# Optimization experiments

Measured on AMD Instinct MI355X. Metric: run time of the kernel, lower is better.

The kernel has to match this reference:

```python
import jax, jax.numpy as jnp
import numpy as np

B, S, D, H = 2, 4096, 256, 4
DH = D // H  # head dim = 64


def setup_inputs() -> dict:
    key = jax.random.key(0)
    ks = jax.random.split(key, 7)
    scale = 1.0 / np.sqrt(D)
    return {
        "x": jax.random.normal(ks[0], (B, S, D), dtype=jnp.float32),
        "Wq": jax.random.normal(ks[1], (D, D), dtype=jnp.float32) * scale,
        "bq": jax.random.normal(ks[2], (D,), dtype=jnp.float32) * scale,
        "Wk": jax.random.normal(ks[3], (D, D), dtype=jnp.float32) * scale,
        "bk": jax.random.normal(ks[4], (D,), dtype=jnp.float32) * scale,
        "Wv": jax.random.normal(ks[5], (D, D), dtype=jnp.float32) * scale,
        "bv": jax.random.normal(ks[6], (D,), dtype=jnp.float32) * scale,
    }


def reference(x, Wq, bq, Wk, bk, Wv, bv):
    b, s, d = x.shape
    # torch Linear: y = x @ W.T + b ; W stored as [out, in]
    q = (jnp.einsum('bsd,ed->bse', x, Wq) + bq).reshape(b, s, H, DH)
    k = (jnp.einsum('bsd,ed->bse', x, Wk) + bk).reshape(b, s, H, DH)
    v = (jnp.einsum('bsd,ed->bse', x, Wv) + bv).reshape(b, s, H, DH)
    # scores: [b, s(query), t(key), h]
    scores = jnp.einsum('bshd,bthd->bsth', q, k) / jnp.sqrt(jnp.float32(DH))
    # softmax over key axis t (dim=-2 in torch layout bsth)
    weights = jax.nn.softmax(scores, axis=2)
    out = jnp.einsum('bsth,bthd->bshd', weights, v)
    return out.reshape(b, s, d)
```

## Files before the change

kernel.cpp:

```cpp
#include <hip/hip_runtime.h>

#define S_LEN 4096
#define D_MODEL 256
#define NH 4
#define DH 64
#define CSC 0.18033688011112042f

typedef __attribute__((ext_vector_type(8))) short bf16x8;
typedef __attribute__((ext_vector_type(8))) unsigned short u16x8;
typedef __attribute__((ext_vector_type(4))) float f32x4;
typedef __attribute__((ext_vector_type(16))) float f32x16;
typedef __attribute__((ext_vector_type(2))) unsigned int u32x2;
typedef __attribute__((ext_vector_type(4))) unsigned int u32x4;

#define MFMA16(a, b, c) __builtin_amdgcn_mfma_f32_16x16x32_bf16((a), (b), (c), 0, 0, 0)
#define MFMA32(a, b, c) __builtin_amdgcn_mfma_f32_32x32x16_bf16((a), (b), (c), 0, 0, 0)
#define SWZ(r, c) ((c) ^ (((r) & 7) << 3))

static __device__ __forceinline__ unsigned short f2bf(float f) {
  unsigned int u = __float_as_uint(f);
  u += 0x7fffu + ((u >> 16) & 1u);
  return (unsigned short)(u >> 16);
}

static __device__ __forceinline__ unsigned int pack2(float lo, float hi) {
  return ((unsigned int)f2bf(hi) << 16) | (unsigned int)f2bf(lo);
}

static __device__ __forceinline__ unsigned int cvtpk(float lo, float hi) {
  unsigned int r;
  asm("v_cvt_pk_bf16_f32 %0, %1, %2" : "=v"(r) : "v"(lo), "v"(hi));
  return r;
}

static __device__ __forceinline__ u16x8 cvt8(float4 a, float4 b) {
  u16x8 v;
  v[0] = f2bf(a.x); v[1] = f2bf(a.y); v[2] = f2bf(a.z); v[3] = f2bf(a.w);
  v[4] = f2bf(b.x); v[5] = f2bf(b.y); v[6] = f2bf(b.z); v[7] = f2bf(b.w);
  return v;
}

__global__ __launch_bounds__(256) void prep(
    const float* __restrict__ Wq, const float* __restrict__ Wk,
    const float* __restrict__ Wv, unsigned short* __restrict__ Wb)
{
  const int gid = blockIdx.x * 256 + threadIdx.x;
  const int l   = gid & 63;
  const int f   = gid >> 6;
  const int kk  = f & 7;
  const int ctn = f >> 3;
  const int ct  = ctn & 3, nt = ctn >> 2;
  const int pj  = nt >> 2, h = nt & 3;
  const float* Wsel = (pj == 0) ? Wq : (pj == 1) ? Wk : Wv;
  const float* src =
      Wsel + (size_t)(h * 64 + ct * 16 + (l & 15)) * D_MODEL + kk * 32 + (l >> 4) * 8;
  float4 a = *(const float4*)src;
  float4 b = *(const float4*)(src + 4);
  *(u16x8*)(Wb + (size_t)gid * 8) = cvt8(a, b);
}

__global__ __launch_bounds__(256) void qkv_proj(
    const float* __restrict__ x, const unsigned short* __restrict__ Wb,
    const float* __restrict__ bq, const float* __restrict__ bk,
    const float* __restrict__ bv,
    unsigned short* __restrict__ Qh, unsigned short* __restrict__ Kh,
    unsigned short* __restrict__ Vt)
{
  __shared__ unsigned short xs[32][264];

  const int tid  = threadIdx.x;
  const int lane = tid & 63;
  const int w    = tid >> 6;
  const int r16  = lane & 15;
  const int hi   = lane >> 4;
  const int m0   = (blockIdx.x >> 1) * 32;
  const int ntB  = (blockIdx.x & 1) * 6;

  {
    const int r  = tid >> 3;
    const int c0 = (tid & 7) * 32;
    const float* xp = x + (size_t)(m0 + r) * D_MODEL + c0;
#pragma unroll
    for (int i = 0; i < 32; i += 8) {
      float4 a = *(const float4*)(xp + i);
      float4 b = *(const float4*)(xp + i + 4);
      *(u16x8*)&xs[r][c0 + i] = cvt8(a, b);
    }
  }
  __syncthreads();

  const int bb = m0 >> 12;
  const int s_base = m0 & 4095;

#pragma unroll
  for (int t = 0; t < 6; ++t) {
    const int nt = ntB + t, pj = nt >> 2, h = nt & 3;
    f32x4 acc[2] = {};
    const size_t fb = (size_t)(nt * 4 + w) * 8;
#pragma unroll
    for (int kk = 0; kk < 8; ++kk) {
      bf16x8 bw = *(const bf16x8*)(Wb + (fb + kk) * 512 + lane * 8);
#pragma unroll
      for (int rt = 0; rt < 2; ++rt) {
        bf16x8 af = *(const bf16x8*)&xs[rt * 16 + r16][kk * 32 + hi * 8];
        acc[rt] = MFMA16(af, bw, acc[rt]);
      }
    }
    const float* bsel = (pj == 0) ? bq : (pj == 1) ? bk : bv;
    const float bias = bsel[h * 64 + w * 16 + r16];

    if (pj < 2) {
      unsigned short* dst = (pj == 0) ? Qh : Kh;
      const float sc = (pj == 0) ? CSC : 1.0f;
#pragma unroll
      for (int rt = 0; rt < 2; ++rt)
#pragma unroll
        for (int j = 0; j < 4; ++j) {
          int s = s_base + rt * 16 + hi * 4 + j;
          dst[((size_t)(bb * NH + h) * S_LEN + s) * DH + w * 16 + r16] =
              f2bf((acc[rt][j] + bias) * sc);
        }
    } else {
      unsigned short* dst = Vt + ((size_t)(bb * NH + h) * DH + w * 16 + r16) * S_LEN;
#pragma unroll
      for (int rt = 0; rt < 2; ++rt) {
        int s0 = s_base + rt * 16 + hi * 4;
        uint2 uu;
        uu.x = pack2(acc[rt][0] + bias, acc[rt][1] + bias);
        uu.y = pack2(acc[rt][2] + bias, acc[rt][3] + bias);
        *(uint2*)(dst + s0) = uu;
      }
    }
  }
}

__global__ __launch_bounds__(512) void attn(
    const unsigned short* __restrict__ Qh,
    const unsigned short* __restrict__ Kh,
    const unsigned short* __restrict__ Vt,
    float* __restrict__ out)
{
  __shared__ unsigned short Ks[2][2][64][64];
  __shared__ unsigned short Vs[2][2][64][64];

  const int tid = threadIdx.x;
  const int ln  = tid & 63;
  const int wv  = tid >> 6;
  const int g   = wv >> 2;
  const int wq  = wv & 3;
  const int r32 = ln & 31;
  const int h   = ln >> 5;

  const int bid = blockIdx.x;
  const int bh  = bid & 7;
  const int q0  = (bid >> 3) * 128;

  const unsigned short* Qb = Qh + (size_t)bh * S_LEN * DH;
  const unsigned short* Kb = Kh + (size_t)bh * S_LEN * DH;
  const unsigned short* Vb = Vt + (size_t)bh * DH * S_LEN;

  const int q = q0 + wq * 32 + r32;
  bf16x8 qf[4];
#pragma unroll
  for (int s = 0; s < 4; ++s)
    qf[s] = *(const bf16x8*)(Qb + (size_t)q * DH + s * 16 + h * 8);

  f32x16 o0 = {}, o1 = {};
  float l_run = 0.f;

  const int p  = tid >> 8;
  const int u  = tid & 255;
  const int sr = u >> 2;
  const int sc = (u & 3) * 16;

  uint4 kA, kB, vA, vB;
  {
    const unsigned short* kp = Kb + ((size_t)(p * 64 + sr)) * DH + sc;
    kA = *(const uint4*)kp;  kB = *(const uint4*)(kp + 8);
    const unsigned short* vp = Vb + (size_t)sr * S_LEN + p * 64 + sc;
    vA = *(const uint4*)vp;  vB = *(const uint4*)(vp + 8);
  }
  *(uint4*)&Ks[0][p][sr][SWZ(sr, sc)]     = kA;
  *(uint4*)&Ks[0][p][sr][SWZ(sr, sc + 8)] = kB;
  *(uint4*)&Vs[0][p][sr][SWZ(sr, sc)]     = vA;
  *(uint4*)&Vs[0][p][sr][SWZ(sr, sc + 8)] = vB;
  {
    const int c = 2 + p;
    const unsigned short* kp = Kb + ((size_t)(c * 64 + sr)) * DH + sc;
    kA = *(const uint4*)kp;  kB = *(const uint4*)(kp + 8);
    const unsigned short* vp = Vb + (size_t)sr * S_LEN + c * 64 + sc;
    vA = *(const uint4*)vp;  vB = *(const uint4*)(vp + 8);
  }

  for (int it = 0; it < 32; ++it) {
    __syncthreads();
    if (it < 31) {
      const int nb = (it + 1) & 1;
      *(uint4*)&Ks[nb][p][sr][SWZ(sr, sc)]     = kA;
      *(uint4*)&Ks[nb][p][sr][SWZ(sr, sc + 8)] = kB;
      *(uint4*)&Vs[nb][p][sr][SWZ(sr, sc)]     = vA;
      *(uint4*)&Vs[nb][p][sr][SWZ(sr, sc + 8)] = vB;
      int c = 2 * (it + 2) + p;  if (c > 63) c = 63;
      const unsigned short* kp = Kb + ((size_t)(c * 64 + sr)) * DH + sc;
      kA = *(const uint4*)kp;  kB = *(const uint4*)(kp + 8);
      const unsigned short* vp = Vb + (size_t)sr * S_LEN + c * 64 + sc;
      vA = *(const uint4*)vp;  vB = *(const uint4*)(vp + 8);
    }
    const int tb = it & 1;

    f32x16 s0 = {}, s1 = {};
    __builtin_amdgcn_s_setprio(1);
#pragma unroll
    for (int s = 0; s < 4; ++s) {
      bf16x8 a0 = *(const bf16x8*)&Ks[tb][g][r32][SWZ(r32, s * 16 + h * 8)];
      bf16x8 a1 = *(const bf16x8*)&Ks[tb][g][32 + r32][SWZ(r32, s * 16 + h * 8)];
      s0 = MFMA32(a0, qf[s], s0);
      s1 = MFMA32(a1, qf[s], s1);
    }
    __builtin_amdgcn_s_setprio(0);

    float ps = 0.f;
#pragma unroll
    for (int i = 0; i < 16; ++i) {
      s0[i] = __builtin_amdgcn_exp2f(s0[i]);  ps += s0[i];
      s1[i] = __builtin_amdgcn_exp2f(s1[i]);  ps += s1[i];
    }
    l_run += ps;

    unsigned int u0[8], u1[8];
#pragma unroll
    for (int gg = 0; gg < 4; ++gg) {
      u0[gg * 2 + 0] = cvtpk(s0[4 * gg + 0], s0[4 * gg + 1]);
      u0[gg * 2 + 1] = cvtpk(s0[4 * gg + 2], s0[4 * gg + 3]);
      u1[gg * 2 + 0] = cvtpk(s1[4 * gg + 0], s1[4 * gg + 1]);
      u1[gg * 2 + 1] = cvtpk(s1[4 * gg + 2], s1[4 * gg + 3]);
    }
    bf16x8 pb[4];
#pragma unroll
    for (int S = 0; S < 2; ++S) {
      u32x2 w0 = __builtin_amdgcn_permlane32_swap(u0[4 * S + 0], u0[4 * S + 2], false, false);
      u32x2 w1 = __builtin_amdgcn_permlane32_swap(u0[4 * S + 1], u0[4 * S + 3], false, false);
      u32x4 t0; t0[0] = w0[0]; t0[1] = w1[0]; t0[2] = w0[1]; t0[3] = w1[1];
      pb[S] = __builtin_bit_cast(bf16x8, t0);
      u32x2 w2 = __builtin_amdgcn_permlane32_swap(u1[4 * S + 0], u1[4 * S + 2], false, false);
      u32x2 w3 = __builtin_amdgcn_permlane32_swap(u1[4 * S + 1], u1[4 * S + 3], false, false);
      u32x4 t1; t1[0] = w2[0]; t1[1] = w3[0]; t1[2] = w2[1]; t1[3] = w3[1];
      pb[2 + S] = __builtin_bit_cast(bf16x8, t1);
    }

    __builtin_amdgcn_s_setprio(1);
#pragma unroll
    for (int s = 0; s < 4; ++s) {
      bf16x8 a0 = *(const bf16x8*)&Vs[tb][g][r32][SWZ(r32, s * 16 + h * 8)];
      bf16x8 a1 = *(const bf16x8*)&Vs[tb][g][32 + r32][SWZ(r32, s * 16 + h * 8)];
      o0 = MFMA32(a0, pb[s], o0);
      o1 = MFMA32(a1, pb[s], o1);
    }
    __builtin_amdgcn_s_setprio(0);
  }

  __syncthreads();
  float* cb = (float*)&Ks[0][0][0][0];
  const int cbase = wq * 64 + ln;
  if (g == 1) {
#pragma unroll
    for (int i = 0; i < 16; ++i) cb[i * 256 + cbase] = o0[i];
    cb[16 * 256 + cbase] = l_run;
  }
  __syncthreads();
  if (g == 0) {
#pragma unroll
    for (int i = 0; i < 16; ++i) o0[i] += cb[i * 256 + cbase];
    l_run += cb[16 * 256 + cbase];
  }
  __syncthreads();
  if (g == 1) {
#pragma unroll
    for (int i = 0; i < 16; ++i) cb[i * 256 + cbase] = o1[i];
  }
  __syncthreads();
  if (g == 0) {
#pragma unroll
    for (int i = 0; i < 16; ++i) o1[i] += cb[i * 256 + cbase];

    const float lt  = l_run + __shfl_xor(l_run, 32);
    const float inv = 1.f / lt;
    const int bb = bh >> 2, hd = bh & 3;
    float* op = out + ((size_t)(bb * S_LEN + q)) * D_MODEL + hd * DH;
#pragma unroll
    for (int gg = 0; gg < 4; ++gg) {
      float4 v0, v1;
      v0.x = o0[4 * gg + 0] * inv;  v0.y = o0[4 * gg + 1] * inv;
      v0.z = o0[4 * gg + 2] * inv;  v0.w = o0[4 * gg + 3] * inv;
      *(float4*)(op + 8 * gg + 4 * h) = v0;
      v1.x = o1[4 * gg + 0] * inv;  v1.y = o1[4 * gg + 1] * inv;
      v1.z = o1[4 * gg + 2] * inv;  v1.w = o1[4 * gg + 3] * inv;
      *(float4*)(op + 32 + 8 * gg + 4 * h) = v1;
    }
  }
}

extern "C" void kernel_launch(void* const* d_in, const int* in_sizes, int n_in,
                              void* d_out, int out_size, void* d_ws, size_t ws_size,
                              hipStream_t stream) {
  const float* x  = (const float*)d_in[0];
  const float* Wq = (const float*)d_in[1];
  const float* bq = (const float*)d_in[2];
  const float* Wk = (const float*)d_in[3];
  const float* bk = (const float*)d_in[4];
  const float* Wv = (const float*)d_in[5];
  const float* bv = (const float*)d_in[6];
  float* out = (float*)d_out;

  const size_t per = (size_t)2 * NH * S_LEN * DH;
  if (ws_size < 3 * per * sizeof(unsigned short)) return;
  unsigned short* Qh = (unsigned short*)d_ws;
  unsigned short* Kh = Qh + per;
  unsigned short* Vt = Kh + per;
  unsigned short* Wb = (unsigned short*)d_out;

  prep<<<96, 256, 0, stream>>>(Wq, Wk, Wv, Wb);
  qkv_proj<<<512, 256, 0, stream>>>(x, Wb, bq, bk, bv, Qh, Kh, Vt);
  attn<<<256, 512, 0, stream>>>(Qh, Kh, Vt, out);
}
```

Before: 66.98 us.

## Split attention KV loop across four wave groups with 1024-thread blocks

Doubles the attention block to 1024 threads so four wave groups each process a quarter of the key/value tiles, halving the per-group loop trip count. K/V staging moves into one combined shared buffer, and each thread now loads a single tile per stage. The final cross-group reduction becomes a two-level tree through shared memory with a padded stride of 33 floats to avoid bank conflicts. This adds waves to hide latency, at the cost of more register pressure under the 1024-thread launch bound and a longer reduction at the end.

```diff
diff --git a/kernel.cpp b/kernel.cpp
--- a/kernel.cpp
+++ b/kernel.cpp
@@ -134,14 +134,13 @@
   }
 }
 
-__global__ __launch_bounds__(512) void attn(
+__global__ __launch_bounds__(1024) void attn(
     const unsigned short* __restrict__ Qh,
     const unsigned short* __restrict__ Kh,
     const unsigned short* __restrict__ Vt,
     float* __restrict__ out)
 {
-  __shared__ unsigned short Ks[2][2][64][64];
-  __shared__ unsigned short Vs[2][2][64][64];
+  __shared__ unsigned short KVs[2][2][4][64][64];
 
   const int tid = threadIdx.x;
   const int ln  = tid & 63;
@@ -168,39 +167,38 @@
   f32x16 o0 = {}, o1 = {};
   float l_run = 0.f;
 
-  const int p  = tid >> 8;
   const int u  = tid & 255;
   const int sr = u >> 2;
   const int sc = (u & 3) * 16;
 
   uint4 kA, kB, vA, vB;
   {
-    const unsigned short* kp = Kb + ((size_t)(p * 64 + sr)) * DH + sc;
+    const unsigned short* kp = Kb + ((size_t)(g * 64 + sr)) * DH + sc;
     kA = *(const uint4*)kp;  kB = *(const uint4*)(kp + 8);
-    const unsigned short* vp = Vb + (size_t)sr * S_LEN + p * 64 + sc;
+    const unsigned short* vp = Vb + (size_t)sr * S_LEN + g * 64 + sc;
     vA = *(const uint4*)vp;  vB = *(const uint4*)(vp + 8);
   }
-  *(uint4*)&Ks[0][p][sr][SWZ(sr, sc)]     = kA;
-  *(uint4*)&Ks[0][p][sr][SWZ(sr, sc + 8)] = kB;
-  *(uint4*)&Vs[0][p][sr][SWZ(sr, sc)]     = vA;
-  *(uint4*)&Vs[0][p][sr][SWZ(sr, sc + 8)] = vB;
+  *(uint4*)&KVs[0][0][g][sr][SWZ(sr, sc)]     = kA;
+  *(uint4*)&KVs[0][0][g][sr][SWZ(sr, sc + 8)] = kB;
+  *(uint4*)&KVs[1][0][g][sr][SWZ(sr, sc)]     = vA;
+  *(uint4*)&KVs[1][0][g][sr][SWZ(sr, sc + 8)] = vB;
   {
-    const int c = 2 + p;
+    const int c = 4 + g;
     const unsigned short* kp = Kb + ((size_t)(c * 64 + sr)) * DH + sc;
     kA = *(const uint4*)kp;  kB = *(const uint4*)(kp + 8);
     const unsigned short* vp = Vb + (size_t)sr * S_LEN + c * 64 + sc;
     vA = *(const uint4*)vp;  vB = *(const uint4*)(vp + 8);
   }
 
-  for (int it = 0; it < 32; ++it) {
+  for (int it = 0; it < 16; ++it) {
     __syncthreads();
-    if (it < 31) {
+    if (it < 15) {
       const int nb = (it + 1) & 1;
-      *(uint4*)&Ks[nb][p][sr][SWZ(sr, sc)]     = kA;
-      *(uint4*)&Ks[nb][p][sr][SWZ(sr, sc + 8)] = kB;
-      *(uint4*)&Vs[nb][p][sr][SWZ(sr, sc)]     = vA;
-      *(uint4*)&Vs[nb][p][sr][SWZ(sr, sc + 8)] = vB;
-      int c = 2 * (it + 2) + p;  if (c > 63) c = 63;
+      *(uint4*)&KVs[0][nb][g][sr][SWZ(sr, sc)]     = kA;
+      *(uint4*)&KVs[0][nb][g][sr][SWZ(sr, sc + 8)] = kB;
+      *(uint4*)&KVs[1][nb][g][sr][SWZ(sr, sc)]     = vA;
+      *(uint4*)&KVs[1][nb][g][sr][SWZ(sr, sc + 8)] = vB;
+      int c = 4 * (it + 2) + g;  if (c > 63) c = 63;
       const unsigned short* kp = Kb + ((size_t)(c * 64 + sr)) * DH + sc;
       kA = *(const uint4*)kp;  kB = *(const uint4*)(kp + 8);
       const unsigned short* vp = Vb + (size_t)sr * S_LEN + c * 64 + sc;
@@ -212,8 +210,8 @@
     __builtin_amdgcn_s_setprio(1);
 #pragma unroll
     for (int s = 0; s < 4; ++s) {
-      bf16x8 a0 = *(const bf16x8*)&Ks[tb][g][r32][SWZ(r32, s * 16 + h * 8)];
-      bf16x8 a1 = *(const bf16x8*)&Ks[tb][g][32 + r32][SWZ(r32, s * 16 + h * 8)];
+      bf16x8 a0 = *(const bf16x8*)&KVs[0][tb][g][r32][SWZ(r32, s * 16 + h * 8)];
+      bf16x8 a1 = *(const bf16x8*)&KVs[0][tb][g][32 + r32][SWZ(r32, s * 16 + h * 8)];
       s0 = MFMA32(a0, qf[s], s0);
       s1 = MFMA32(a1, qf[s], s1);
     }
@@ -251,8 +249,8 @@
     __builtin_amdgcn_s_setprio(1);
 #pragma unroll
     for (int s = 0; s < 4; ++s) {
-      bf16x8 a0 = *(const bf16x8*)&Vs[tb][g][r32][SWZ(r32, s * 16 + h * 8)];
-      bf16x8 a1 = *(const bf16x8*)&Vs[tb][g][32 + r32][SWZ(r32, s * 16 + h * 8)];
+      bf16x8 a0 = *(const bf16x8*)&KVs[1][tb][g][r32][SWZ(r32, s * 16 + h * 8)];
+      bf16x8 a1 = *(const bf16x8*)&KVs[1][tb][g][32 + r32][SWZ(r32, s * 16 + h * 8)];
       o0 = MFMA32(a0, pb[s], o0);
       o1 = MFMA32(a1, pb[s], o1);
     }
@@ -260,28 +258,35 @@
   }
 
   __syncthreads();
-  float* cb = (float*)&Ks[0][0][0][0];
+  float* cb = (float*)&KVs[0][0][0][0][0];
   const int cbase = wq * 64 + ln;
+
+  if (g >= 2) {
+    const int base = ((g - 2) * 256 + cbase) * 33;
+#pragma unroll
+    for (int i = 0; i < 16; ++i) { cb[base + i] = o0[i]; cb[base + 16 + i] = o1[i]; }
+    cb[base + 32] = l_run;
+  }
+  __syncthreads();
+  if (g < 2) {
+    const int base = (g * 256 + cbase) * 33;
+#pragma unroll
+    for (int i = 0; i < 16; ++i) { o0[i] += cb[base + i]; o1[i] += cb[base + 16 + i]; }
+    l_run += cb[base + 32];
+  }
+  __syncthreads();
   if (g == 1) {
-#pragma unroll
-    for (int i = 0; i < 16; ++i) cb[i * 256 + cbase] = o0[i];
-    cb[16 * 256 + cbase] = l_run;
+    const int base = cbase * 33;
+#pragma unroll
+    for (int i = 0; i < 16; ++i) { cb[base + i] = o0[i]; cb[base + 16 + i] = o1[i]; }
+    cb[base + 32] = l_run;
   }
   __syncthreads();
   if (g == 0) {
-#pragma unroll
-    for (int i = 0; i < 16; ++i) o0[i] += cb[i * 256 + cbase];
-    l_run += cb[16 * 256 + cbase];
-  }
-  __syncthreads();
-  if (g == 1) {
-#pragma unroll
-    for (int i = 0; i < 16; ++i) cb[i * 256 + cbase] = o1[i];
-  }
-  __syncthreads();
-  if (g == 0) {
-#pragma unroll
-    for (int i = 0; i < 16; ++i) o1[i] += cb[i * 256 + cbase];
+    const int base = cbase * 33;
+#pragma unroll
+    for (int i = 0; i < 16; ++i) { o0[i] += cb[base + i]; o1[i] += cb[base + 16 + i]; }
+    l_run += cb[base + 32];
 
     const float lt  = l_run + __shfl_xor(l_run, 32);
     const float inv = 1.f / lt;
@@ -321,5 +326,5 @@
 
   prep<<<96, 256, 0, stream>>>(Wq, Wk, Wv, Wb);
   qkv_proj<<<512, 256, 0, stream>>>(x, Wb, bq, bk, bv, Qh, Kh, Vt);
-  attn<<<256, 512, 0, stream>>>(Qh, Kh, Vt, out);
-}
+  attn<<<256, 1024, 0, stream>>>(Qh, Kh, Vt, out);
+}
```

Result: faster. 65.41 us (-2.3%).

## Restructure attention into 4-way key split with 2 query tiles per wave and fragment-major LDS

Applied to the files above, without the earlier changes.

Each attention wave now handles two 32-query tiles against a quarter of each 256-key chunk, so every K/V fragment read from LDS feeds two MFMAs. K/V are staged in a padded, fragment-major LDS layout instead of the XOR swizzle. The cross-wave reduction becomes a two-stage tree. The QKV projection now goes through an LDS transpose buffer so Q/K/V stores are coalesced 16-byte writes. This raises register pressure (launch bounds 512,2) and adds extra syncs in the projection in exchange for less LDS traffic per MFMA and better global store coalescing.

```diff
diff --git a/kernel.cpp b/kernel.cpp
--- a/kernel.cpp
+++ b/kernel.cpp
@@ -5,6 +5,7 @@
 #define NH 4
 #define DH 64
 #define CSC 0.18033688011112042f
+#define FRAG 520
 
 typedef __attribute__((ext_vector_type(8))) short bf16x8;
 typedef __attribute__((ext_vector_type(8))) unsigned short u16x8;
@@ -15,16 +16,11 @@
 
 #define MFMA16(a, b, c) __builtin_amdgcn_mfma_f32_16x16x32_bf16((a), (b), (c), 0, 0, 0)
 #define MFMA32(a, b, c) __builtin_amdgcn_mfma_f32_32x32x16_bf16((a), (b), (c), 0, 0, 0)
-#define SWZ(r, c) ((c) ^ (((r) & 7) << 3))
 
 static __device__ __forceinline__ unsigned short f2bf(float f) {
   unsigned int u = __float_as_uint(f);
   u += 0x7fffu + ((u >> 16) & 1u);
   return (unsigned short)(u >> 16);
-}
-
-static __device__ __forceinline__ unsigned int pack2(float lo, float hi) {
-  return ((unsigned int)f2bf(hi) << 16) | (unsigned int)f2bf(lo);
 }
 
 static __device__ __forceinline__ unsigned int cvtpk(float lo, float hi) {
@@ -38,6 +34,29 @@
   v[0] = f2bf(a.x); v[1] = f2bf(a.y); v[2] = f2bf(a.z); v[3] = f2bf(a.w);
   v[4] = f2bf(b.x); v[5] = f2bf(b.y); v[6] = f2bf(b.z); v[7] = f2bf(b.w);
   return v;
+}
+
+static __device__ __forceinline__ void pack_pb(const f32x16& s0, const f32x16& s1,
+                                               bf16x8* pb) {
+  unsigned int u0[8], u1[8];
+#pragma unroll
+  for (int gg = 0; gg < 4; ++gg) {
+    u0[gg * 2 + 0] = cvtpk(s0[4 * gg + 0], s0[4 * gg + 1]);
+    u0[gg * 2 + 1] = cvtpk(s0[4 * gg + 2], s0[4 * gg + 3]);
+    u1[gg * 2 + 0] = cvtpk(s1[4 * gg + 0], s1[4 * gg + 1]);
+    u1[gg * 2 + 1] = cvtpk(s1[4 * gg + 2], s1[4 * gg + 3]);
+  }
+#pragma unroll
+  for (int S = 0; S < 2; ++S) {
+    u32x2 w0 = __builtin_amdgcn_permlane32_swap(u0[4 * S + 0], u0[4 * S + 2], false, false);
+    u32x2 w1 = __builtin_amdgcn_permlane32_swap(u0[4 * S + 1], u0[4 * S + 3], false, false);
+    u32x4 t0; t0[0] = w0[0]; t0[1] = w1[0]; t0[2] = w0[1]; t0[3] = w1[1];
+    pb[S] = __builtin_bit_cast(bf16x8, t0);
+    u32x2 w2 = __builtin_amdgcn_permlane32_swap(u1[4 * S + 0], u1[4 * S + 2], false, false);
+    u32x2 w3 = __builtin_amdgcn_permlane32_swap(u1[4 * S + 1], u1[4 * S + 3], false, false);
+    u32x4 t1; t1[0] = w2[0]; t1[1] = w3[0]; t1[2] = w2[1]; t1[3] = w3[1];
+    pb[2 + S] = __builtin_bit_cast(bf16x8, t1);
+  }
 }
 
 __global__ __launch_bounds__(256) void prep(
@@ -67,6 +86,7 @@
     unsigned short* __restrict__ Vt)
 {
   __shared__ unsigned short xs[32][264];
+  __shared__ float tbuf[32][68];
 
   const int tid  = threadIdx.x;
   const int lane = tid & 63;
@@ -92,7 +112,6 @@
   const int bb = m0 >> 12;
   const int s_base = m0 & 4095;
 
-#pragma unroll
   for (int t = 0; t < 6; ++t) {
     const int nt = ntB + t, pj = nt >> 2, h = nt & 3;
     f32x4 acc[2] = {};
@@ -108,46 +127,48 @@
     }
     const float* bsel = (pj == 0) ? bq : (pj == 1) ? bk : bv;
     const float bias = bsel[h * 64 + w * 16 + r16];
+    const float scl  = (pj == 0) ? CSC : 1.0f;
+
+#pragma unroll
+    for (int rt = 0; rt < 2; ++rt)
+#pragma unroll
+      for (int j = 0; j < 4; ++j)
+        tbuf[rt * 16 + hi * 4 + j][w * 16 + r16] = (acc[rt][j] + bias) * scl;
+    __syncthreads();
 
     if (pj < 2) {
-      unsigned short* dst = (pj == 0) ? Qh : Kh;
-      const float sc = (pj == 0) ? CSC : 1.0f;
-#pragma unroll
-      for (int rt = 0; rt < 2; ++rt)
-#pragma unroll
-        for (int j = 0; j < 4; ++j) {
-          int s = s_base + rt * 16 + hi * 4 + j;
-          dst[((size_t)(bb * NH + h) * S_LEN + s) * DH + w * 16 + r16] =
-              f2bf((acc[rt][j] + bias) * sc);
-        }
+      const int s_l = tid >> 3, c0 = (tid & 7) * 8;
+      float4 a = *(const float4*)&tbuf[s_l][c0];
+      float4 b = *(const float4*)&tbuf[s_l][c0 + 4];
+      unsigned short* dst = ((pj == 0) ? Qh : Kh) +
+          ((size_t)(bb * NH + h) * S_LEN + s_base + s_l) * DH + c0;
+      *(u16x8*)dst = cvt8(a, b);
     } else {
-      unsigned short* dst = Vt + ((size_t)(bb * NH + h) * DH + w * 16 + r16) * S_LEN;
-#pragma unroll
-      for (int rt = 0; rt < 2; ++rt) {
-        int s0 = s_base + rt * 16 + hi * 4;
-        uint2 uu;
-        uu.x = pack2(acc[rt][0] + bias, acc[rt][1] + bias);
-        uu.y = pack2(acc[rt][2] + bias, acc[rt][3] + bias);
-        *(uint2*)(dst + s0) = uu;
-      }
-    }
-  }
-}
-
-__global__ __launch_bounds__(512) void attn(
+      const int d_l = tid & 63, sblk = (tid >> 6) * 8;
+      u16x8 vv;
+#pragma unroll
+      for (int e = 0; e < 8; ++e) vv[e] = f2bf(tbuf[sblk + e][d_l]);
+      unsigned short* dst = Vt +
+          ((size_t)(bb * NH + h) * DH + d_l) * S_LEN + s_base + sblk;
+      *(u16x8*)dst = vv;
+    }
+    __syncthreads();
+  }
+}
+
+__global__ __launch_bounds__(512, 2) void attn(
     const unsigned short* __restrict__ Qh,
     const unsigned short* __restrict__ Kh,
     const unsigned short* __restrict__ Vt,
     float* __restrict__ out)
 {
-  __shared__ unsigned short Ks[2][2][64][64];
-  __shared__ unsigned short Vs[2][2][64][64];
+  __shared__ unsigned short KV[2][2][4][8 * FRAG];
 
   const int tid = threadIdx.x;
   const int ln  = tid & 63;
   const int wv  = tid >> 6;
-  const int g   = wv >> 2;
-  const int wq  = wv & 3;
+  const int g   = wv >> 1;
+  const int qw  = wv & 1;
   const int r32 = ln & 31;
   const int h   = ln >> 5;
 
@@ -159,143 +180,166 @@
   const unsigned short* Kb = Kh + (size_t)bh * S_LEN * DH;
   const unsigned short* Vb = Vt + (size_t)bh * DH * S_LEN;
 
-  const int q = q0 + wq * 32 + r32;
-  bf16x8 qf[4];
-#pragma unroll
-  for (int s = 0; s < 4; ++s)
-    qf[s] = *(const bf16x8*)(Qb + (size_t)q * DH + s * 16 + h * 8);
-
-  f32x16 o0 = {}, o1 = {};
-  float l_run = 0.f;
-
-  const int p  = tid >> 8;
-  const int u  = tid & 255;
-  const int sr = u >> 2;
-  const int sc = (u & 3) * 16;
-
-  uint4 kA, kB, vA, vB;
-  {
-    const unsigned short* kp = Kb + ((size_t)(p * 64 + sr)) * DH + sc;
-    kA = *(const uint4*)kp;  kB = *(const uint4*)(kp + 8);
-    const unsigned short* vp = Vb + (size_t)sr * S_LEN + p * 64 + sc;
-    vA = *(const uint4*)vp;  vB = *(const uint4*)(vp + 8);
-  }
-  *(uint4*)&Ks[0][p][sr][SWZ(sr, sc)]     = kA;
-  *(uint4*)&Ks[0][p][sr][SWZ(sr, sc + 8)] = kB;
-  *(uint4*)&Vs[0][p][sr][SWZ(sr, sc)]     = vA;
-  *(uint4*)&Vs[0][p][sr][SWZ(sr, sc + 8)] = vB;
-  {
-    const int c = 2 + p;
-    const unsigned short* kp = Kb + ((size_t)(c * 64 + sr)) * DH + sc;
-    kA = *(const uint4*)kp;  kB = *(const uint4*)(kp + 8);
-    const unsigned short* vp = Vb + (size_t)sr * S_LEN + c * 64 + sc;
-    vA = *(const uint4*)vp;  vB = *(const uint4*)(vp + 8);
-  }
-
-  for (int it = 0; it < 32; ++it) {
+  bf16x8 qf[2][4];
+#pragma unroll
+  for (int qt = 0; qt < 2; ++qt) {
+    const int q = q0 + qw * 64 + qt * 32 + r32;
+#pragma unroll
+    for (int s = 0; s < 4; ++s)
+      qf[qt][s] = *(const bf16x8*)(Qb + (size_t)q * DH + s * 16 + h * 8);
+  }
+
+  f32x16 o[2][2] = {};
+  float l_run[2] = {0.f, 0.f};
+
+  const int v   = tid & 127;
+  const int gs  = tid >> 7;
+  const int sr  = v >> 1;
+  const int sc  = (v & 1) * 32;
+  int off[4];
+#pragma unroll
+  for (int m = 0; m < 4; ++m) {
+    const int d0 = sc + 8 * m;
+    const int f  = (d0 >> 4) * 2 + (sr >> 5);
+    const int la = (sr & 31) + 32 * ((d0 >> 3) & 1);
+    off[m] = f * FRAG + la * 8;
+  }
+
+  uint4 kst[4], vst[4];
+#define LOAD_CHUNK(c)                                                          \
+  { const uint4* kp = (const uint4*)(Kb + ((size_t)(c) * 64 + sr) * DH + sc);  \
+    kst[0] = kp[0]; kst[1] = kp[1]; kst[2] = kp[2]; kst[3] = kp[3];            \
+    const uint4* vp = (const uint4*)(Vb + (size_t)sr * S_LEN + (c) * 64 + sc); \
+    vst[0] = vp[0]; vst[1] = vp[1]; vst[2] = vp[2]; vst[3] = vp[3]; }
+#define STAGE(par)                                                             \
+  { _Pragma("unroll")                                                          \
+    for (int m = 0; m < 4; ++m) {                                              \
+      *(uint4*)&KV[par][0][gs][off[m]] = kst[m];                               \
+      *(uint4*)&KV[par][1][gs][off[m]] = vst[m];                               \
+    } }
+
+  LOAD_CHUNK(gs);
+  STAGE(0);
+  LOAD_CHUNK(4 + gs);
+
+  for (int it = 0; it < 16; ++it) {
     __syncthreads();
-    if (it < 31) {
-      const int nb = (it + 1) & 1;
-      *(uint4*)&Ks[nb][p][sr][SWZ(sr, sc)]     = kA;
-      *(uint4*)&Ks[nb][p][sr][SWZ(sr, sc + 8)] = kB;
-      *(uint4*)&Vs[nb][p][sr][SWZ(sr, sc)]     = vA;
-      *(uint4*)&Vs[nb][p][sr][SWZ(sr, sc + 8)] = vB;
-      int c = 2 * (it + 2) + p;  if (c > 63) c = 63;
-      const unsigned short* kp = Kb + ((size_t)(c * 64 + sr)) * DH + sc;
-      kA = *(const uint4*)kp;  kB = *(const uint4*)(kp + 8);
-      const unsigned short* vp = Vb + (size_t)sr * S_LEN + c * 64 + sc;
-      vA = *(const uint4*)vp;  vB = *(const uint4*)(vp + 8);
-    }
-    const int tb = it & 1;
-
-    f32x16 s0 = {}, s1 = {};
+    if (it < 15) {
+      STAGE((it + 1) & 1);
+      int c = 4 * (it + 2) + gs;  if (c > 63) c = 63;
+      LOAD_CHUNK(c);
+    }
+    const unsigned short* Kc = &KV[it & 1][0][g][0];
+    const unsigned short* Vc = &KV[it & 1][1][g][0];
+    const int lb = ln * 8;
+
+    f32x16 s00 = {}, s01 = {}, s10 = {}, s11 = {};
     __builtin_amdgcn_s_setprio(1);
 #pragma unroll
     for (int s = 0; s < 4; ++s) {
-      bf16x8 a0 = *(const bf16x8*)&Ks[tb][g][r32][SWZ(r32, s * 16 + h * 8)];
-      bf16x8 a1 = *(const bf16x8*)&Ks[tb][g][32 + r32][SWZ(r32, s * 16 + h * 8)];
-      s0 = MFMA32(a0, qf[s], s0);
-      s1 = MFMA32(a1, qf[s], s1);
+      bf16x8 a0 = *(const bf16x8*)(Kc + lb + (s * 2 + 0) * FRAG);
+      bf16x8 a1 = *(const bf16x8*)(Kc + lb + (s * 2 + 1) * FRAG);
+      s00 = MFMA32(a0, qf[0][s], s00);
+      s01 = MFMA32(a1, qf[0][s], s01);
+      s10 = MFMA32(a0, qf[1][s], s10);
+      s11 = MFMA32(a1, qf[1][s], s11);
     }
     __builtin_amdgcn_s_setprio(0);
 
-    float ps = 0.f;
+    bf16x8 pb0[4], pb1[4];
+    {
+      float ps = 0.f;
+#pragma unroll
+      for (int i = 0; i < 16; ++i) {
+        s00[i] = __builtin_amdgcn_exp2f(s00[i]);  ps += s00[i];
+        s01[i] = __builtin_amdgcn_exp2f(s01[i]);  ps += s01[i];
+      }
+      l_run[0] += ps;
+      pack_pb(s00, s01, pb0);
+    }
+    {
+      float ps = 0.f;
+#pragma unroll
+      for (int i = 0; i < 16; ++i) {
+        s10[i] = __builtin_amdgcn_exp2f(s10[i]);  ps += s10[i];
+        s11[i] = __builtin_amdgcn_exp2f(s11[i]);  ps += s11[i];
+      }
+      l_run[1] += ps;
+      pack_pb(s10, s11, pb1);
+    }
+
+    __builtin_amdgcn_s_setprio(1);
+#pragma unroll
+    for (int s = 0; s < 4; ++s) {
+      bf16x8 b0 = *(const bf16x8*)(Vc + lb + (s * 2 + 0) * FRAG);
+      bf16x8 b1 = *(const bf16x8*)(Vc + lb + (s * 2 + 1) * FRAG);
+      o[0][0] = MFMA32(b0, pb0[s], o[0][0]);
+      o[0][1] = MFMA32(b1, pb0[s], o[0][1]);
+      o[1][0] = MFMA32(b0, pb1[s], o[1][0]);
+      o[1][1] = MFMA32(b1, pb1[s], o[1][1]);
+    }
+    __builtin_amdgcn_s_setprio(0);
+  }
+
+  __syncthreads();
+  float* cb = (float*)&KV[0][0][0][0];
+
+  if (wv >= 4) {
+    const int base = ((wv - 4) * 64 + ln) * 68;
 #pragma unroll
     for (int i = 0; i < 16; ++i) {
-      s0[i] = __builtin_amdgcn_exp2f(s0[i]);  ps += s0[i];
-      s1[i] = __builtin_amdgcn_exp2f(s1[i]);  ps += s1[i];
-    }
-    l_run += ps;
-
-    unsigned int u0[8], u1[8];
-#pragma unroll
-    for (int gg = 0; gg < 4; ++gg) {
-      u0[gg * 2 + 0] = cvtpk(s0[4 * gg + 0], s0[4 * gg + 1]);
-      u0[gg * 2 + 1] = cvtpk(s0[4 * gg + 2], s0[4 * gg + 3]);
-      u1[gg * 2 + 0] = cvtpk(s1[4 * gg + 0], s1[4 * gg + 1]);
-      u1[gg * 2 + 1] = cvtpk(s1[4 * gg + 2], s1[4 * gg + 3]);
-    }
-    bf16x8 pb[4];
-#pragma unroll
-    for (int S = 0; S < 2; ++S) {
-      u32x2 w0 = __builtin_amdgcn_permlane32_swap(u0[4 * S + 0], u0[4 * S + 2], false, false);
-      u32x2 w1 = __builtin_amdgcn_permlane32_swap(u0[4 * S + 1], u0[4 * S + 3], false, false);
-      u32x4 t0; t0[0] = w0[0]; t0[1] = w1[0]; t0[2] = w0[1]; t0[3] = w1[1];
-      pb[S] = __builtin_bit_cast(bf16x8, t0);
-      u32x2 w2 = __builtin_amdgcn_permlane32_swap(u1[4 * S + 0], u1[4 * S + 2], false, false);
-      u32x2 w3 = __builtin_amdgcn_permlane32_swap(u1[4 * S + 1], u1[4 * S + 3], false, false);
-      u32x4 t1; t1[0] = w2[0]; t1[1] = w3[0]; t1[2] = w2[1]; t1[3] = w3[1];
-      pb[2 + S] = __builtin_bit_cast(bf16x8, t1);
-    }
-
-    __builtin_amdgcn_s_setprio(1);
-#pragma unroll
-    for (int s = 0; s < 4; ++s) {
-      bf16x8 a0 = *(const bf16x8*)&Vs[tb][g][r32][SWZ(r32, s * 16 + h * 8)];
-      bf16x8 a1 = *(const bf16x8*)&Vs[tb][g][32 + r32][SWZ(r32, s * 16 + h * 8)];
-      o0 = MFMA32(a0, pb[s], o0);
-      o1 = MFMA32(a1, pb[s], o1);
-    }
-    __builtin_amdgcn_s_setprio(0);
-  }
-
-  __syncthreads();
-  float* cb = (float*)&Ks[0][0][0][0];
-  const int cbase = wq * 64 + ln;
-  if (g == 1) {
-#pragma unroll
-    for (int i = 0; i < 16; ++i) cb[i * 256 + cbase] = o0[i];
-    cb[16 * 256 + cbase] = l_run;
-  }
-  __syncthreads();
-  if (g == 0) {
-#pragma unroll
-    for (int i = 0; i < 16; ++i) o0[i] += cb[i * 256 + cbase];
-    l_run += cb[16 * 256 + cbase];
-  }
-  __syncthreads();
-  if (g == 1) {
-#pragma unroll
-    for (int i = 0; i < 16; ++i) cb[i * 256 + cbase] = o1[i];
-  }
-  __syncthreads();
-  if (g == 0) {
-#pragma unroll
-    for (int i = 0; i < 16; ++i) o1[i] += cb[i * 256 + cbase];
-
-    const float lt  = l_run + __shfl_xor(l_run, 32);
-    const float inv = 1.f / lt;
+      cb[base + i]      = o[0][0][i];  cb[base + 16 + i] = o[0][1][i];
+      cb[base + 32 + i] = o[1][0][i];  cb[base + 48 + i] = o[1][1][i];
+    }
+    cb[base + 64] = l_run[0];  cb[base + 65] = l_run[1];
+  }
+  __syncthreads();
+  if (wv < 4) {
+    const int base = (wv * 64 + ln) * 68;
+#pragma unroll
+    for (int i = 0; i < 16; ++i) {
+      o[0][0][i] += cb[base + i];       o[0][1][i] += cb[base + 16 + i];
+      o[1][0][i] += cb[base + 32 + i];  o[1][1][i] += cb[base + 48 + i];
+    }
+    l_run[0] += cb[base + 64];  l_run[1] += cb[base + 65];
+  }
+  __syncthreads();
+  if (wv == 2 || wv == 3) {
+    const int base = ((wv - 2) * 64 + ln) * 68;
+#pragma unroll
+    for (int i = 0; i < 16; ++i) {
+      cb[base + i]      = o[0][0][i];  cb[base + 16 + i] = o[0][1][i];
+      cb[base + 32 + i] = o[1][0][i];  cb[base + 48 + i] = o[1][1][i];
+    }
+    cb[base + 64] = l_run[0];  cb[base + 65] = l_run[1];
+  }
+  __syncthreads();
+  if (wv < 2) {
+    const int base = (wv * 64 + ln) * 68;
+#pragma unroll
+    for (int i = 0; i < 16; ++i) {
+      o[0][0][i] += cb[base + i];       o[0][1][i] += cb[base + 16 + i];
+      o[1][0][i] += cb[base + 32 + i];  o[1][1][i] += cb[base + 48 + i];
+    }
+    l_run[0] += cb[base + 64];  l_run[1] += cb[base + 65];
+
     const int bb = bh >> 2, hd = bh & 3;
-    float* op = out + ((size_t)(bb * S_LEN + q)) * D_MODEL + hd * DH;
-#pragma unroll
-    for (int gg = 0; gg < 4; ++gg) {
-      float4 v0, v1;
-      v0.x = o0[4 * gg + 0] * inv;  v0.y = o0[4 * gg + 1] * inv;
-      v0.z = o0[4 * gg + 2] * inv;  v0.w = o0[4 * gg + 3] * inv;
-      *(float4*)(op + 8 * gg + 4 * h) = v0;
-      v1.x = o1[4 * gg + 0] * inv;  v1.y = o1[4 * gg + 1] * inv;
-      v1.z = o1[4 * gg + 2] * inv;  v1.w = o1[4 * gg + 3] * inv;
-      *(float4*)(op + 32 + 8 * gg + 4 * h) = v1;
+#pragma unroll
+    for (int qt = 0; qt < 2; ++qt) {
+      const float lt  = l_run[qt] + __shfl_xor(l_run[qt], 32);
+      const float inv = 1.f / lt;
+      const int q = q0 + wv * 64 + qt * 32 + r32;
+      float* op = out + ((size_t)(bb * S_LEN + q)) * D_MODEL + hd * DH;
+#pragma unroll
+      for (int gg = 0; gg < 4; ++gg) {
+        float4 v0, v1;
+        v0.x = o[qt][0][4 * gg + 0] * inv;  v0.y = o[qt][0][4 * gg + 1] * inv;
+        v0.z = o[qt][0][4 * gg + 2] * inv;  v0.w = o[qt][0][4 * gg + 3] * inv;
+        *(float4*)(op + 8 * gg + 4 * h) = v0;
+        v1.x = o[qt][1][4 * gg + 0] * inv;  v1.y = o[qt][1][4 * gg + 1] * inv;
+        v1.z = o[qt][1][4 * gg + 2] * inv;  v1.w = o[qt][1][4 * gg + 3] * inv;
+        *(float4*)(op + 32 + 8 * gg + 4 * h) = v1;
+      }
     }
   }
 }
```

After: 109.0 us. 62.7% more time.
